# Kernel optimization log

Hardware: AMD Instinct MI355X
Metric: run time of the kernel (lower is better)

The kernel has to match this reference:

```python
import jax, jax.numpy as jnp
import numpy as np

B, T, D = 4, 50, 512
SRC, SENTS, WORDS = 400, 16, 40
NEG = jnp.float32(-1e30)  # stands in for -inf mask fill (numerically identical post-softmax)


def _seq_mask(lengths, max_len):
    # [n, max_len] bool, True where position < length
    return jnp.arange(max_len)[None, :] < lengths[:, None]


def _mlp_score(q, h, Wq, bq, Uc, v):
    # Bahdanau additive score: v^T tanh(W q + U h)
    # q: [b,t,d], h: [b,s,d] -> [b,t,s]
    wq = q @ Wq + bq                       # [b,t,d]
    uh = h @ Uc                            # [b,s,d]
    wquh = jnp.tanh(wq[:, :, None, :] + uh[:, None, :, :])  # [b,t,s,d]
    return jnp.einsum('btsd,d->bts', wquh, v)


def setup_inputs() -> dict:
    key = jax.random.key(0)
    ks = jax.random.split(key, 20)
    s = np.float32(1.0 / np.sqrt(D))
    def p(k, shape):
        return jax.random.normal(k, shape, jnp.float32) * s
    return {
        'source': jax.random.normal(ks[0], (B, T, D), jnp.float32),
        'src_bank': jax.random.normal(ks[1], (SRC, B, D), jnp.float32),
        'src_lengths': jax.random.randint(ks[2], (B,), 1, SRC + 1),
        'qa_sent_bank': jax.random.normal(ks[3], (SENTS, B, D), jnp.float32),
        'qa_sent_lengths': jax.random.randint(ks[4], (B,), 1, SENTS + 1),
        'qa_word_bank': jax.random.normal(ks[5], (WORDS, B, SENTS, D), jnp.float32),
        'qa_word_lengths': jax.random.randint(ks[6], (B, SENTS), 1, WORDS + 1),
        'Wq_word': p(ks[7], (D, D)), 'bq_word': jnp.zeros((D,), jnp.float32),
        'Uc_word': p(ks[8], (D, D)), 'v_word': p(ks[9], (D,)),
        'Wq_sent': p(ks[10], (D, D)), 'bq_sent': jnp.zeros((D,), jnp.float32),
        'Uc_sent': p(ks[11], (D, D)), 'v_sent': p(ks[12], (D,)),
        'Wq_pass': p(ks[13], (D, D)), 'bq_pass': jnp.zeros((D,), jnp.float32),
        'Uc_pass': p(ks[14], (D, D)), 'v_pass': p(ks[15], (D,)),
    }


def _forward(source, src_bank, qa_sent_bank, qa_word_bank,
             Wq_word, bq_word, Uc_word, v_word,
             Wq_sent, bq_sent, Uc_sent, v_sent,
             Wq_pass, bq_pass, Uc_pass, v_pass,
             src_lengths, qa_word_lengths):
    b = source.shape[0]
    # [words,b,sents,d] -> [b,sents,words,d] -> [b, sents*words, d]
    qa_word = jnp.transpose(qa_word_bank, (1, 2, 0, 3)).reshape(b, SENTS * WORDS, D)
    src = jnp.transpose(src_bank, (1, 0, 2))       # [b,src,d]
    sent = jnp.transpose(qa_sent_bank, (1, 0, 2))  # [b,sents,d]

    qa_word_align = _mlp_score(source, qa_word, Wq_word, bq_word, Uc_word, v_word)  # [b,t,sents*words]
    src_align = _mlp_score(source, src, Wq_pass, bq_pass, Uc_pass, v_pass)          # [b,t,src]
    qa_sent_align = _mlp_score(source, sent, Wq_sent, bq_sent, Uc_sent, v_sent)     # [b,t,sents]

    # hierarchical combination: word score scaled by its sentence score
    qa_hier = (qa_word_align.reshape(b, T, SENTS, WORDS)
               * qa_sent_align[..., None]).reshape(b, T, SENTS * WORDS)

    align = jnp.concatenate([src_align, qa_hier], axis=-1)  # [b,t,src+sents*words]

    qa_mask = _seq_mask(qa_word_lengths.reshape(-1), WORDS).reshape(b, SENTS * WORDS)[:, None, :]
    src_mask = _seq_mask(src_lengths, SRC)[:, None, :]
    mask = jnp.concatenate([src_mask, qa_mask], axis=-1)

    align = jnp.where(mask, align, NEG)
    align_vectors = jax.nn.softmax(align, axis=-1)  # joint length-masked softmax

    memory = jnp.concatenate([src, qa_word], axis=1)          # [b, src+sents*words, d]
    c = jnp.einsum('bts,bsd->btd', align_vectors, memory)     # weighted context sum
    return c


def reference(source, src_bank, src_lengths, qa_sent_bank, qa_sent_lengths,
              qa_word_bank, qa_word_lengths,
              Wq_word, bq_word, Uc_word, v_word,
              Wq_sent, bq_sent, Uc_sent, v_sent,
              Wq_pass, bq_pass, Uc_pass, v_pass):
    # qa_sent_lengths is accepted but unused, matching the original forward()
    return _forward(source, src_bank, qa_sent_bank, qa_word_bank,
                    Wq_word, bq_word, Uc_word, v_word,
                    Wq_sent, bq_sent, Uc_sent, v_sent,
                    Wq_pass, bq_pass, Uc_pass, v_pass,
                    src_lengths, qa_word_lengths)
```

## Files before the change

kernel.cpp:

```cpp
#include <hip/hip_runtime.h>
#include <hip/hip_bf16.h>


#define B_    4
#define T_    50
#define D_    512
#define SRC_  400
#define SENTS_ 16
#define WORDS_ 40
#define NW_   640
#define NMEM_ 1040
#define NK_   1056
#define NJOB_ 1056

#define C2L2E 2.8853900817779268f

typedef unsigned short ushort_t;
using s8v = __attribute__((ext_vector_type(8))) short;
using f4v = __attribute__((ext_vector_type(4))) float;

#define OFF_WQ_WORD 0
#define OFF_WQ_SENT 102400
#define OFF_WQ_PASS 204800
#define OFF_UH_SRC  307200
#define OFF_UH_WORD 1126400
#define OFF_UH_SENT 2437120
#define OFF_SC_SRC  2469888
#define OFF_SC_WORD 2549888
#define OFF_SC_SENT 2677888
#define P_BYTE_OFF  10724352ull
#define MT_BYTE_OFF 11265024ull

__device__ __forceinline__ ushort_t f2b(float f) {
    __hip_bfloat16 h = __float2bfloat16(f);
    return *(ushort_t*)&h;
}

__global__ __launch_bounds__(256) void kA(
    const float* __restrict__ source, const float* __restrict__ src_bank,
    const float* __restrict__ qa_sent_bank, const float* __restrict__ qa_word_bank,
    const float* __restrict__ w0, const float* __restrict__ w1,
    const float* __restrict__ w2, const float* __restrict__ w3,
    const float* __restrict__ w4, const float* __restrict__ w5,
    const float* __restrict__ bq_word, const float* __restrict__ bq_sent,
    const float* __restrict__ bq_pass,
    float* __restrict__ wsf, ushort_t* __restrict__ mt)
{
    __shared__ float smemf[4224];
    int bid = blockIdx.x;
    int tid = threadIdx.x;

    if (bid >= 624) {
        int tb = bid - 624;
        int b = tb / 528, r = tb - b * 528;
        int s0 = (r % 33) * 32, d0 = (r / 33) * 32;
        float (*tile)[33] = (float(*)[33])smemf;
        int tx = tid & 31, ty = tid >> 5;
#pragma unroll
        for (int a = 0; a < 4; ++a) {
            int s = s0 + ty + a * 8;
            float val = 0.f;
            if (s < SRC_) {
                val = src_bank[(s * B_ + b) * D_ + d0 + tx];
            } else if (s < NMEM_) {
                int j = s - SRC_; int se = j / WORDS_; int wd = j - se * WORDS_;
                val = qa_word_bank[((wd * B_ + b) * SENTS_ + se) * D_ + d0 + tx];
            }
            tile[ty + a * 8][tx] = val;
        }
        __syncthreads();
        ushort_t* base = mt + (size_t)b * D_ * NK_;
#pragma unroll
        for (int a = 0; a < 4; ++a) {
            int d = d0 + ty + a * 8;
            base[(size_t)d * NK_ + s0 + tx] = f2b(tile[tx][ty + a * 8]);
        }
        return;
    }

    int z, rem;
    if (bid < 96)       { z = bid >> 5; rem = bid & 31; }
    else if (bid < 416) { z = 3; rem = bid - 96; }
    else if (bid < 616) { z = 4; rem = bid - 416; }
    else                { z = 5; rem = bid - 616; }
    int by = rem >> 3, bx = rem & 7;
    int M, atype; const float* bias; const float* W; float* C;
    switch (z) {
        case 0: M = 200;  atype = 0; bias = bq_word; W = w0; C = wsf + OFF_WQ_WORD; break;
        case 1: M = 200;  atype = 0; bias = bq_sent; W = w1; C = wsf + OFF_WQ_SENT; break;
        case 2: M = 200;  atype = 0; bias = bq_pass; W = w2; C = wsf + OFF_WQ_PASS; break;
        case 3: M = 2560; atype = 1; bias = nullptr; W = w3; C = wsf + OFF_UH_WORD; break;
        case 4: M = 1600; atype = 2; bias = nullptr; W = w4; C = wsf + OFF_UH_SRC;  break;
        default: M = 64;  atype = 3; bias = nullptr; W = w5; C = wsf + OFF_UH_SENT; break;
    }
    int m0 = by * 64, n0 = bx * 64;

    int lane = tid & 63, wvx = tid >> 6, quad = lane >> 4, l16 = lane & 15;
    int sm = tid >> 2, koff = (tid & 3) * 8;
    int rW = tid >> 3, cW = (tid & 7) * 8;
    int rWs = rW * 68 + (cW ^ (((rW >> 3) & 3) << 4));
    int nB = tid >> 2, kB8 = (tid & 3) * 8;
    int colp = nB ^ (((kB8 >> 3) & 3) << 4);

    short* At = (short*)smemf;
    short* Bt = (short*)(smemf + 1024);
    float* Wtmp = smemf + 2048;

    const float* arow = nullptr;
    {
        int rr = m0 + sm;
        if (rr < M) {
            if (atype == 0) arow = source + rr * D_;
            else if (atype == 1) { int b = rr / NW_; int j = rr - b * NW_;
                                   int se = j / WORDS_; int wd = j - se * WORDS_;
                                   arow = qa_word_bank + ((wd * B_ + b) * SENTS_ + se) * D_; }
            else if (atype == 2) { int b = rr / SRC_; int j = rr - b * SRC_;
                                   arow = src_bank + (j * B_ + b) * D_; }
            else                 { int b = rr >> 4; int s2 = rr & 15;
                                   arow = qa_sent_bank + (s2 * B_ + b) * D_; }
        }
    }
    const float* wbase = W + n0 + cW;

    auto loadA = [&](float* r, int kk) {
        if (arow) {
            float4 f0 = *(const float4*)(arow + kk * 32 + koff);
            float4 f1 = *(const float4*)(arow + kk * 32 + koff + 4);
            r[0]=f0.x; r[1]=f0.y; r[2]=f0.z; r[3]=f0.w;
            r[4]=f1.x; r[5]=f1.y; r[6]=f1.z; r[7]=f1.w;
        } else {
#pragma unroll
            for (int i = 0; i < 8; ++i) r[i] = 0.f;
        }
    };
    auto loadW = [&](float* r, int kk) {
        const float* p = wbase + (kk * 32 + rW) * D_;
        float4 f0 = *(const float4*)p;
        float4 f1 = *(const float4*)(p + 4);
        r[0]=f0.x; r[1]=f0.y; r[2]=f0.z; r[3]=f0.w;
        r[4]=f1.x; r[5]=f1.y; r[6]=f1.z; r[7]=f1.w;
    };
    auto storeWtmp = [&](const float* r) {
        *(float4*)(Wtmp + rWs)     = float4{r[0], r[1], r[2], r[3]};
        *(float4*)(Wtmp + rWs + 4) = float4{r[4], r[5], r[6], r[7]};
    };
    auto storeAt = [&](const float* r) {
        union { ushort_t u[8]; int4 v; } pk;
#pragma unroll
        for (int i = 0; i < 8; ++i) pk.u[i] = f2b(r[i]);
        *(int4*)(At + sm * 32 + koff) = pk.v;
    };
    auto buildBt = [&]() {
        union { ushort_t u[8]; int4 v; } pk;
#pragma unroll
        for (int i = 0; i < 8; ++i) pk.u[i] = f2b(Wtmp[(kB8 + i) * 68 + colp]);
        *(int4*)(Bt + nB * 32 + kB8) = pk.v;
    };

    f4v acc[4] = { {0.f,0.f,0.f,0.f}, {0.f,0.f,0.f,0.f},
                   {0.f,0.f,0.f,0.f}, {0.f,0.f,0.f,0.f} };

    float ac[8], an[8], wn[8];
    loadA(ac, 0);
    {
        float w0r[8];
        loadW(w0r, 0);
        storeWtmp(w0r);
    }
    loadW(wn, 1);
    loadA(an, 1);
    __syncthreads();

    for (int kk = 0; kk < 16; ++kk) {
        storeAt(ac);
        buildBt();
        __syncthreads();
        if (kk < 15) storeWtmp(wn);
        if (kk < 14) loadW(wn, kk + 2);
        if (kk < 15) {
#pragma unroll
            for (int i = 0; i < 8; ++i) ac[i] = an[i];
        }
        if (kk < 14) loadA(an, kk + 2);
        s8v af = *(const s8v*)(At + (wvx * 16 + l16) * 32 + quad * 8);
#pragma unroll
        for (int ng = 0; ng < 4; ++ng) {
            s8v bf = *(const s8v*)(Bt + (ng * 16 + l16) * 32 + quad * 8);
            acc[ng] = __builtin_amdgcn_mfma_f32_16x16x32_bf16(af, bf, acc[ng], 0, 0, 0);
        }
        __syncthreads();
    }

#pragma unroll
    for (int ng = 0; ng < 4; ++ng) {
        int col = n0 + ng * 16 + l16;
        float bb = bias ? bias[col] : 0.f;
#pragma unroll
        for (int rr2 = 0; rr2 < 4; ++rr2) {
            int row = m0 + wvx * 16 + quad * 4 + rr2;
            if (row < M) C[row * D_ + col] = (acc[ng][rr2] + bb) * C2L2E;
        }
    }
}

__global__ __launch_bounds__(256) void k2_scores(
    const float* __restrict__ v_word, const float* __restrict__ v_sent,
    const float* __restrict__ v_pass,
    const int* __restrict__ src_lengths, const int* __restrict__ qa_word_lengths,
    float* __restrict__ wsf)
{
    int lane = threadIdx.x & 63;
    int jid = blockIdx.x * 4 + (threadIdx.x >> 6);
    int job = jid / 5, fifth = jid - job * 5;
    int b = job / NJOB_, slot = job - b * NJOB_;
    const float* uh; const float* v; const float* wq; float* out; int ostride;
    if (slot < SRC_) {
        if (slot >= src_lengths[b]) return;
        uh = wsf + OFF_UH_SRC + (size_t)(b * SRC_ + slot) * D_;
        v = v_pass; wq = wsf + OFF_WQ_PASS + b * T_ * D_;
        out = wsf + OFF_SC_SRC + b * T_ * SRC_ + slot; ostride = SRC_;
    } else if (slot < NMEM_) {
        int j = slot - SRC_;
        int se = j / WORDS_; int wd = j - se * WORDS_;
        if (wd >= qa_word_lengths[b * SENTS_ + se]) return;
        uh = wsf + OFF_UH_WORD + (size_t)(b * NW_ + j) * D_;
        v = v_word; wq = wsf + OFF_WQ_WORD + b * T_ * D_;
        out = wsf + OFF_SC_WORD + b * T_ * NW_ + j; ostride = NW_;
    } else {
        int s2 = slot - NMEM_;
        uh = wsf + OFF_UH_SENT + (size_t)(b * SENTS_ + s2) * D_;
        v = v_sent; wq = wsf + OFF_WQ_SENT + b * T_ * D_;
        out = wsf + OFF_SC_SENT + b * T_ * SENTS_ + s2; ostride = SENTS_;
    }
    int d0 = lane * 8;
    float4 u0 = *(const float4*)(uh + d0);
    float4 u1 = *(const float4*)(uh + d0 + 4);
    float uhr[8] = {u0.x, u0.y, u0.z, u0.w, u1.x, u1.y, u1.z, u1.w};
    float4 v0 = *(const float4*)(v + d0);
    float4 v1 = *(const float4*)(v + d0 + 4);
    float vr[8] = {v0.x, v0.y, v0.z, v0.w, v1.x, v1.y, v1.z, v1.w};

    float vs = ((vr[0] + vr[1]) + (vr[2] + vr[3])) + ((vr[4] + vr[5]) + (vr[6] + vr[7]));
#pragma unroll
    for (int off = 32; off > 0; off >>= 1) vs += __shfl_xor(vs, off, 64);

    const float* wqh = wq + (fifth * 10) * D_ + d0;
    int tbase = fifth * 10;
#pragma unroll 1
    for (int g = 0; g < 2; ++g) {
        float a5[5];
#pragma unroll
        for (int u5 = 0; u5 < 5; ++u5) {
            const float* wr = wqh + (g * 5 + u5) * D_;
            float4 w0 = *(const float4*)(wr);
            float4 w1 = *(const float4*)(wr + 4);
            float wrr[8] = {w0.x, w0.y, w0.z, w0.w, w1.x, w1.y, w1.z, w1.w};
            float a = 0.f;
#pragma unroll
            for (int j = 0; j < 8; ++j) {
                float e = __builtin_amdgcn_exp2f(wrr[j] + uhr[j]);
                float r = __builtin_amdgcn_rcpf(e + 1.f);
                a = fmaf(vr[j], r, a);
            }
            a5[u5] = a;
        }
#pragma unroll
        for (int off = 32; off > 0; off >>= 1) {
#pragma unroll
            for (int u5 = 0; u5 < 5; ++u5) a5[u5] += __shfl_xor(a5[u5], off, 64);
        }
        if (lane == 0) {
#pragma unroll
            for (int u5 = 0; u5 < 5; ++u5)
                out[(tbase + g * 5 + u5) * ostride] = fmaf(-2.f, a5[u5], vs);
        }
    }
}

__global__ __launch_bounds__(256) void k3a_softmax(
    const int* __restrict__ src_lengths, const int* __restrict__ qa_word_lengths,
    const float* __restrict__ wsf, ushort_t* __restrict__ P)
{
    __shared__ float p[NMEM_];
    __shared__ float red[4];
    int tid = threadIdx.x, lane = tid & 63, wv = tid >> 6;
    int bt = blockIdx.x, b = bt / T_, t = bt - b * T_;
    const float* sc_src  = wsf + OFF_SC_SRC  + bt * SRC_;
    const float* sc_word = wsf + OFF_SC_WORD + bt * NW_;
    const float* sc_sent = wsf + OFF_SC_SENT + bt * SENTS_;
    int slen = src_lengths[b];
    float mx = -3.0e38f;
    for (int j = tid; j < NMEM_; j += 256) {
        float val;
        if (j < SRC_) {
            val = (j < slen) ? sc_src[j] : -1e30f;
        } else {
            int jj = j - SRC_; int se = jj / WORDS_; int wd = jj - se * WORDS_;
            float raw = sc_word[jj] * sc_sent[se];
            val = (wd < qa_word_lengths[b * SENTS_ + se]) ? raw : -1e30f;
        }
        p[j] = val;
        mx = fmaxf(mx, val);
    }
#pragma unroll
    for (int off = 32; off > 0; off >>= 1) mx = fmaxf(mx, __shfl_xor(mx, off, 64));
    if (lane == 0) red[wv] = mx;
    __syncthreads();
    mx = fmaxf(fmaxf(red[0], red[1]), fmaxf(red[2], red[3]));
    __syncthreads();
    float lsum = 0.f;
    for (int j = tid; j < NMEM_; j += 256) {
        float e = __expf(p[j] - mx);
        p[j] = e; lsum += e;
    }
#pragma unroll
    for (int off = 32; off > 0; off >>= 1) lsum += __shfl_xor(lsum, off, 64);
    if (lane == 0) red[wv] = lsum;
    __syncthreads();
    float inv = 1.f / (red[0] + red[1] + red[2] + red[3]);
    ushort_t* prow = P + (size_t)(b * 64 + t) * NK_;
    for (int j = tid; j < NK_; j += 256)
        prow[j] = (j < NMEM_) ? f2b(p[j] * inv) : (ushort_t)0;
}

__global__ __launch_bounds__(256) void k3c_gemm(
    const ushort_t* __restrict__ P, const ushort_t* __restrict__ Mt,
    float* __restrict__ out)
{
    __shared__ short At[64 * 32];
    __shared__ short Bt[32 * 32];
    int b = blockIdx.y;
    int n0 = blockIdx.x * 32;
    int tid = threadIdx.x;
    int lane = tid & 63, wv = tid >> 6;
    int quad = lane >> 4, l16 = lane & 15;
    int smA = tid >> 2, koffA = (tid & 3) * 8;
    int smB = tid >> 3, koffB = (tid & 7) * 4;

    const ushort_t* arow = P + (size_t)(b * 64 + smA) * NK_ + koffA;
    const ushort_t* brow = Mt + ((size_t)(b * D_ + n0 + smB)) * NK_ + koffB;

    f4v acc[2] = { {0.f,0.f,0.f,0.f}, {0.f,0.f,0.f,0.f} };

    int4 a0 = *(const int4*)(arow);
    int2 b0 = *(const int2*)(brow);
    int4 a1 = *(const int4*)(arow + 32);
    int2 b1 = *(const int2*)(brow + 32);
    int4 a2 = *(const int4*)(arow + 64);
    int2 b2 = *(const int2*)(brow + 64);

    for (int kk = 0; kk < 33; ++kk) {
        *(int4*)(At + smA * 32 + koffA) = a0;
        *(int2*)(Bt + smB * 32 + koffB) = b0;
        __syncthreads();
        a0 = a1; a1 = a2; b0 = b1; b1 = b2;
        if (kk < 30) {
            a2 = *(const int4*)(arow + (kk + 3) * 32);
            b2 = *(const int2*)(brow + (kk + 3) * 32);
        }
        s8v af = *(const s8v*)(At + (wv * 16 + l16) * 32 + quad * 8);
#pragma unroll
        for (int ng = 0; ng < 2; ++ng) {
            s8v bf = *(const s8v*)(Bt + (ng * 16 + l16) * 32 + quad * 8);
            acc[ng] = __builtin_amdgcn_mfma_f32_16x16x32_bf16(af, bf, acc[ng], 0, 0, 0);
        }
        __syncthreads();
    }
#pragma unroll
    for (int ng = 0; ng < 2; ++ng) {
        int col = n0 + ng * 16 + l16;
#pragma unroll
        for (int rr = 0; rr < 4; ++rr) {
            int row = wv * 16 + quad * 4 + rr;
            if (row < T_) out[(size_t)(b * T_ + row) * D_ + col] = acc[ng][rr];
        }
    }
}

extern "C" void kernel_launch(void* const* d_in, const int* in_sizes, int n_in,
                              void* d_out, int out_size, void* d_ws, size_t ws_size,
                              hipStream_t stream)
{
    (void)in_sizes; (void)n_in; (void)out_size; (void)ws_size;
    const float* source          = (const float*)d_in[0];
    const float* src_bank        = (const float*)d_in[1];
    const int*   src_lengths     = (const int*)d_in[2];
    const float* qa_sent_bank    = (const float*)d_in[3];
    const float* qa_word_bank    = (const float*)d_in[5];
    const int*   qa_word_lengths = (const int*)d_in[6];
    const float* Wq_word = (const float*)d_in[7];
    const float* bq_word = (const float*)d_in[8];
    const float* Uc_word = (const float*)d_in[9];
    const float* v_word  = (const float*)d_in[10];
    const float* Wq_sent = (const float*)d_in[11];
    const float* bq_sent = (const float*)d_in[12];
    const float* Uc_sent = (const float*)d_in[13];
    const float* v_sent  = (const float*)d_in[14];
    const float* Wq_pass = (const float*)d_in[15];
    const float* bq_pass = (const float*)d_in[16];
    const float* Uc_pass = (const float*)d_in[17];
    const float* v_pass  = (const float*)d_in[18];

    float* wsf = (float*)d_ws;
    ushort_t* Pb  = (ushort_t*)((char*)d_ws + P_BYTE_OFF);
    ushort_t* mt  = (ushort_t*)((char*)d_ws + MT_BYTE_OFF);
    float* out = (float*)d_out;

    kA<<<dim3(2736), dim3(256), 0, stream>>>(
        source, src_bank, qa_sent_bank, qa_word_bank,
        Wq_word, Wq_sent, Wq_pass, Uc_word, Uc_pass, Uc_sent,
        bq_word, bq_sent, bq_pass, wsf, mt);
    k2_scores<<<dim3(5280), dim3(256), 0, stream>>>(
        v_word, v_sent, v_pass, src_lengths, qa_word_lengths, wsf);
    k3a_softmax<<<dim3(200), dim3(256), 0, stream>>>(src_lengths, qa_word_lengths, wsf, Pb);
    k3c_gemm<<<dim3(16, 4), dim3(256), 0, stream>>>(Pb, mt, out);
}
```

Before: 154.1 us.

## Fuse softmax with context sum and drop bf16 transpose and MFMA GEMM

Removes the bf16 transposed-memory build from the first kernel and the separate MFMA GEMM. The softmax kernel now computes the weighted context sum itself, reading the fp32 source and word banks in their original layout. It loops only up to each sequence's length, rounded to 4, so masked positions are skipped. This cuts one launch and the transpose and P writes, but each of the 200 (b,t) blocks now re-reads its batch's memory rows through cache with scalar FMAs instead of tensor cores.

```diff
diff --git a/kernel.cpp b/kernel.cpp
--- a/kernel.cpp
+++ b/kernel.cpp
@@ -10,7 +10,6 @@
 #define WORDS_ 40
 #define NW_   640
 #define NMEM_ 1040
-#define NK_   1056
 #define NJOB_ 1056
 
 #define C2L2E 2.8853900817779268f
@@ -28,8 +27,6 @@
 #define OFF_SC_SRC  2469888
 #define OFF_SC_WORD 2549888
 #define OFF_SC_SENT 2677888
-#define P_BYTE_OFF  10724352ull
-#define MT_BYTE_OFF 11265024ull
 
 __device__ __forceinline__ ushort_t f2b(float f) {
     __hip_bfloat16 h = __float2bfloat16(f);
@@ -44,39 +41,11 @@
     const float* __restrict__ w4, const float* __restrict__ w5,
     const float* __restrict__ bq_word, const float* __restrict__ bq_sent,
     const float* __restrict__ bq_pass,
-    float* __restrict__ wsf, ushort_t* __restrict__ mt)
+    float* __restrict__ wsf)
 {
     __shared__ float smemf[4224];
     int bid = blockIdx.x;
     int tid = threadIdx.x;
-
-    if (bid >= 624) {
-        int tb = bid - 624;
-        int b = tb / 528, r = tb - b * 528;
-        int s0 = (r % 33) * 32, d0 = (r / 33) * 32;
-        float (*tile)[33] = (float(*)[33])smemf;
-        int tx = tid & 31, ty = tid >> 5;
-#pragma unroll
-        for (int a = 0; a < 4; ++a) {
-            int s = s0 + ty + a * 8;
-            float val = 0.f;
-            if (s < SRC_) {
-                val = src_bank[(s * B_ + b) * D_ + d0 + tx];
-            } else if (s < NMEM_) {
-                int j = s - SRC_; int se = j / WORDS_; int wd = j - se * WORDS_;
-                val = qa_word_bank[((wd * B_ + b) * SENTS_ + se) * D_ + d0 + tx];
-            }
-            tile[ty + a * 8][tx] = val;
-        }
-        __syncthreads();
-        ushort_t* base = mt + (size_t)b * D_ * NK_;
-#pragma unroll
-        for (int a = 0; a < 4; ++a) {
-            int d = d0 + ty + a * 8;
-            base[(size_t)d * NK_ + s0 + tx] = f2b(tile[tx][ty + a * 8]);
-        }
-        return;
-    }
 
     int z, rem;
     if (bid < 96)       { z = bid >> 5; rem = bid & 31; }
@@ -277,9 +246,11 @@
     }
 }
 
-__global__ __launch_bounds__(256) void k3a_softmax(
+__global__ __launch_bounds__(256) void k3ac(
     const int* __restrict__ src_lengths, const int* __restrict__ qa_word_lengths,
-    const float* __restrict__ wsf, ushort_t* __restrict__ P)
+    const float* __restrict__ wsf,
+    const float* __restrict__ src_bank, const float* __restrict__ qa_word_bank,
+    float* __restrict__ out)
 {
     __shared__ float p[NMEM_];
     __shared__ float red[4];
@@ -289,6 +260,7 @@
     const float* sc_word = wsf + OFF_SC_WORD + bt * NW_;
     const float* sc_sent = wsf + OFF_SC_SENT + bt * SENTS_;
     int slen = src_lengths[b];
+
     float mx = -3.0e38f;
     for (int j = tid; j < NMEM_; j += 256) {
         float val;
@@ -318,63 +290,47 @@
     if (lane == 0) red[wv] = lsum;
     __syncthreads();
     float inv = 1.f / (red[0] + red[1] + red[2] + red[3]);
-    ushort_t* prow = P + (size_t)(b * 64 + t) * NK_;
-    for (int j = tid; j < NK_; j += 256)
-        prow[j] = (j < NMEM_) ? f2b(p[j] * inv) : (ushort_t)0;
-}
-
-__global__ __launch_bounds__(256) void k3c_gemm(
-    const ushort_t* __restrict__ P, const ushort_t* __restrict__ Mt,
-    float* __restrict__ out)
-{
-    __shared__ short At[64 * 32];
-    __shared__ short Bt[32 * 32];
-    int b = blockIdx.y;
-    int n0 = blockIdx.x * 32;
-    int tid = threadIdx.x;
-    int lane = tid & 63, wv = tid >> 6;
-    int quad = lane >> 4, l16 = lane & 15;
-    int smA = tid >> 2, koffA = (tid & 3) * 8;
-    int smB = tid >> 3, koffB = (tid & 7) * 4;
-
-    const ushort_t* arow = P + (size_t)(b * 64 + smA) * NK_ + koffA;
-    const ushort_t* brow = Mt + ((size_t)(b * D_ + n0 + smB)) * NK_ + koffB;
-
-    f4v acc[2] = { {0.f,0.f,0.f,0.f}, {0.f,0.f,0.f,0.f} };
-
-    int4 a0 = *(const int4*)(arow);
-    int2 b0 = *(const int2*)(brow);
-    int4 a1 = *(const int4*)(arow + 32);
-    int2 b1 = *(const int2*)(brow + 32);
-    int4 a2 = *(const int4*)(arow + 64);
-    int2 b2 = *(const int2*)(brow + 64);
-
-    for (int kk = 0; kk < 33; ++kk) {
-        *(int4*)(At + smA * 32 + koffA) = a0;
-        *(int2*)(Bt + smB * 32 + koffB) = b0;
-        __syncthreads();
-        a0 = a1; a1 = a2; b0 = b1; b1 = b2;
-        if (kk < 30) {
-            a2 = *(const int4*)(arow + (kk + 3) * 32);
-            b2 = *(const int2*)(brow + (kk + 3) * 32);
-        }
-        s8v af = *(const s8v*)(At + (wv * 16 + l16) * 32 + quad * 8);
-#pragma unroll
-        for (int ng = 0; ng < 2; ++ng) {
-            s8v bf = *(const s8v*)(Bt + (ng * 16 + l16) * 32 + quad * 8);
-            acc[ng] = __builtin_amdgcn_mfma_f32_16x16x32_bf16(af, bf, acc[ng], 0, 0, 0);
-        }
-        __syncthreads();
-    }
-#pragma unroll
-    for (int ng = 0; ng < 2; ++ng) {
-        int col = n0 + ng * 16 + l16;
-#pragma unroll
-        for (int rr = 0; rr < 4; ++rr) {
-            int row = wv * 16 + quad * 4 + rr;
-            if (row < T_) out[(size_t)(b * T_ + row) * D_ + col] = acc[ng][rr];
-        }
-    }
+    for (int j = tid; j < NMEM_; j += 256) p[j] *= inv;
+    __syncthreads();
+
+    int d0 = tid * 2;
+    float acc0 = 0.f, acc1 = 0.f;
+    {
+        int slen4 = (slen + 3) & ~3;
+        const float* bank = src_bank + (size_t)b * D_ + d0;
+        for (int s = 0; s < slen4; s += 4) {
+            float4 pv = *(const float4*)(p + s);
+            const float* r0 = bank + (size_t)s * (B_ * D_);
+            float2 m0 = *(const float2*)(r0);
+            float2 m1 = *(const float2*)(r0 + B_ * D_);
+            float2 m2 = *(const float2*)(r0 + 2 * B_ * D_);
+            float2 m3 = *(const float2*)(r0 + 3 * B_ * D_);
+            acc0 = fmaf(pv.x, m0.x, acc0); acc1 = fmaf(pv.x, m0.y, acc1);
+            acc0 = fmaf(pv.y, m1.x, acc0); acc1 = fmaf(pv.y, m1.y, acc1);
+            acc0 = fmaf(pv.z, m2.x, acc0); acc1 = fmaf(pv.z, m2.y, acc1);
+            acc0 = fmaf(pv.w, m3.x, acc0); acc1 = fmaf(pv.w, m3.y, acc1);
+        }
+    }
+#pragma unroll 1
+    for (int se = 0; se < SENTS_; ++se) {
+        int lim = qa_word_lengths[b * SENTS_ + se];
+        int lim4 = (lim + 3) & ~3;
+        const float* bank = qa_word_bank + ((size_t)b * SENTS_ + se) * D_ + d0;
+        const float* pw = p + SRC_ + se * WORDS_;
+        for (int wd = 0; wd < lim4; wd += 4) {
+            float4 pv = *(const float4*)(pw + wd);
+            const float* r0 = bank + (size_t)wd * (B_ * SENTS_ * D_);
+            float2 m0 = *(const float2*)(r0);
+            float2 m1 = *(const float2*)(r0 + B_ * SENTS_ * D_);
+            float2 m2 = *(const float2*)(r0 + 2 * B_ * SENTS_ * D_);
+            float2 m3 = *(const float2*)(r0 + 3 * B_ * SENTS_ * D_);
+            acc0 = fmaf(pv.x, m0.x, acc0); acc1 = fmaf(pv.x, m0.y, acc1);
+            acc0 = fmaf(pv.y, m1.x, acc0); acc1 = fmaf(pv.y, m1.y, acc1);
+            acc0 = fmaf(pv.z, m2.x, acc0); acc1 = fmaf(pv.z, m2.y, acc1);
+            acc0 = fmaf(pv.w, m3.x, acc0); acc1 = fmaf(pv.w, m3.y, acc1);
+        }
+    }
+    *(float2*)(out + (size_t)(b * T_ + t) * D_ + d0) = float2{acc0, acc1};
 }
 
 extern "C" void kernel_launch(void* const* d_in, const int* in_sizes, int n_in,
@@ -402,16 +358,14 @@
     const float* v_pass  = (const float*)d_in[18];
 
     float* wsf = (float*)d_ws;
-    ushort_t* Pb  = (ushort_t*)((char*)d_ws + P_BYTE_OFF);
-    ushort_t* mt  = (ushort_t*)((char*)d_ws + MT_BYTE_OFF);
     float* out = (float*)d_out;
 
-    kA<<<dim3(2736), dim3(256), 0, stream>>>(
+    kA<<<dim3(624), dim3(256), 0, stream>>>(
         source, src_bank, qa_sent_bank, qa_word_bank,
         Wq_word, Wq_sent, Wq_pass, Uc_word, Uc_pass, Uc_sent,
-        bq_word, bq_sent, bq_pass, wsf, mt);
+        bq_word, bq_sent, bq_pass, wsf);
     k2_scores<<<dim3(5280), dim3(256), 0, stream>>>(
         v_word, v_sent, v_pass, src_lengths, qa_word_lengths, wsf);
-    k3a_softmax<<<dim3(200), dim3(256), 0, stream>>>(src_lengths, qa_word_lengths, wsf, Pb);
-    k3c_gemm<<<dim3(16, 4), dim3(256), 0, stream>>>(Pb, mt, out);
-}
+    k3ac<<<dim3(200), dim3(256), 0, stream>>>(
+        src_lengths, qa_word_lengths, wsf, src_bank, qa_word_bank, out);
+}
```

Result: slower. 188.3 us (+22.2%).
